# Performance work log

Measured on AMD Instinct MI355X. Metric: run time of the kernel, lower is better.

Reference implementation:

```python
import jax, jax.numpy as jnp
import numpy as np

TEMPERATURE = 0.1
EPS = 1e-12  # matches F.normalize eps clamp


def setup_inputs() -> dict:
    key = jax.random.key(0)
    k1, k2 = jax.random.split(key)
    B, D = 4096, 1024
    z1 = jax.random.normal(k1, (B, D), dtype=jnp.float32)
    z2 = jax.random.normal(k2, (B, D), dtype=jnp.float32)
    return {"z1": z1, "z2": z2}


def reference(z1, z2):
    B = z1.shape[0]
    # L2-normalize rows (F.normalize dim=1, eps clamp)
    n1 = z1 / jnp.maximum(jnp.linalg.norm(z1, axis=1, keepdims=True), EPS)
    n2 = z2 / jnp.maximum(jnp.linalg.norm(z2, axis=1, keepdims=True), EPS)
    reps = jnp.concatenate([n1, n2], axis=0)  # [2B, D]
    # Rows are unit-norm, so cosine similarity == dot product -> one GEMM
    sim = (reps @ reps.T) / TEMPERATURE  # [2B, 2B]
    # positives: diag offsets +B and -B
    pos = jnp.concatenate([jnp.diagonal(sim, B), jnp.diagonal(sim, -B)])  # [2B]
    # logits row i = [pos_i, sim[i, j != i]]. logsumexp over that set =
    # logaddexp(pos_i, logsumexp over the row with the main diagonal removed).
    eye = jnp.eye(2 * B, dtype=bool)
    masked = jnp.where(eye, -jnp.inf, sim)
    lse_neg = jax.scipy.special.logsumexp(masked, axis=1)  # [2B]
    lse = jnp.logaddexp(pos, lse_neg)
    # CrossEntropyLoss with labels==0 -> mean(lse - logit_0) = mean(lse - pos)
    return jnp.mean(lse - pos)
```

## Files before the change

kernel.cpp:

```cpp
#include <hip/hip_runtime.h>

#define D_DIM 1024
#define B_HALF 4096
#define NROWS 8192
#define INV_TEMP 10.0f

typedef __bf16 bf16x8 __attribute__((ext_vector_type(8)));
typedef float floatx4 __attribute__((ext_vector_type(4)));

__device__ __forceinline__ unsigned short f32_to_bf16(float f) {
    union { float f; unsigned u; } v; v.f = f;
    unsigned r = 0x7FFFu + ((v.u >> 16) & 1u);
    return (unsigned short)((v.u + r) >> 16);
}

__global__ __launch_bounds__(256) void normalize_kernel(
    const float* __restrict__ z1, const float* __restrict__ z2,
    unsigned short* __restrict__ R)
{
    const int row = blockIdx.x;
    const int tid = threadIdx.x;
    const float* src = (row < B_HALF) ? (z1 + (size_t)row * D_DIM)
                                      : (z2 + (size_t)(row - B_HALF) * D_DIM);
    float4 v = ((const float4*)src)[tid];
    float ss = v.x * v.x + v.y * v.y + v.z * v.z + v.w * v.w;
    #pragma unroll
    for (int off = 32; off > 0; off >>= 1) ss += __shfl_down(ss, off);
    __shared__ float wsum[4];
    if ((tid & 63) == 0) wsum[tid >> 6] = ss;
    __syncthreads();
    float tot = wsum[0] + wsum[1] + wsum[2] + wsum[3];
    float scale = 1.0f / fmaxf(sqrtf(tot), 1e-12f);
    ushort4 o;
    o.x = f32_to_bf16(v.x * scale);
    o.y = f32_to_bf16(v.y * scale);
    o.z = f32_to_bf16(v.z * scale);
    o.w = f32_to_bf16(v.w * scale);
    ((ushort4*)(R + (size_t)row * D_DIM))[tid] = o;
}

__global__ __launch_bounds__(256) void gemm_lse_kernel(
    const unsigned short* __restrict__ R,
    float* __restrict__ partial, float* __restrict__ pos)
{
    __shared__ unsigned short As[128 * 32];
    __shared__ unsigned short Bs[128 * 32];
    __shared__ float rowsum[2][128];
    __shared__ float colsum[2][128];

    const int t = blockIdx.x;
    int rt = (int)((129.0f - sqrtf((float)(16641 - 8 * t))) * 0.5f);
    while ((rt + 1) * 64 - (rt + 1) * rt / 2 <= t) ++rt;
    while (rt * 64 - rt * (rt - 1) / 2 > t) --rt;
    const int ct = rt + (t - (rt * 64 - rt * (rt - 1) / 2));
    const bool isDiag = (rt == ct);

    const int tid = threadIdx.x;
    const int wave = tid >> 6, lane = tid & 63;
    const int wm = wave >> 1, wn = wave & 1;
    const int row0 = rt * 128, col0 = ct * 128;

    floatx4 acc[4][4] = {};

    const int lrow = lane >> 2;
    const int lk = (lane & 3) * 8;
    const unsigned short* gA = R + (size_t)row0 * D_DIM;
    const unsigned short* gB = R + (size_t)col0 * D_DIM;

    const int lm = lane & 15;
    const int lq = lane >> 4;

    for (int k0 = 0; k0 < D_DIM; k0 += 32) {
        #pragma unroll
        for (int rnd = 0; rnd < 2; ++rnd) {
            const int c = rnd * 4 + wave;
            const int grow = c * 16 + lrow;
            __builtin_amdgcn_global_load_lds(
                (const __attribute__((address_space(1))) unsigned int*)(gA + (size_t)grow * D_DIM + k0 + lk),
                (__attribute__((address_space(3))) unsigned int*)(As + c * 512),
                16, 0, 0);
            __builtin_amdgcn_global_load_lds(
                (const __attribute__((address_space(1))) unsigned int*)(gB + (size_t)grow * D_DIM + k0 + lk),
                (__attribute__((address_space(3))) unsigned int*)(Bs + c * 512),
                16, 0, 0);
        }
        __syncthreads();

        bf16x8 af[4], bfr[4];
        #pragma unroll
        for (int i = 0; i < 4; ++i) {
            af[i]  = *(const bf16x8*)(As + (wm * 64 + i * 16 + lm) * 32 + lq * 8);
            bfr[i] = *(const bf16x8*)(Bs + (wn * 64 + i * 16 + lm) * 32 + lq * 8);
        }
        #pragma unroll
        for (int mi = 0; mi < 4; ++mi)
            #pragma unroll
            for (int ni = 0; ni < 4; ++ni)
                acc[mi][ni] = __builtin_amdgcn_mfma_f32_16x16x32_bf16(
                    af[mi], bfr[ni], acc[mi][ni], 0, 0, 0);
        __syncthreads();
    }

    float ecol[4] = {0.0f, 0.0f, 0.0f, 0.0f};
    #pragma unroll
    for (int mi = 0; mi < 4; ++mi) {
        #pragma unroll
        for (int reg = 0; reg < 4; ++reg) {
            const int gr = row0 + wm * 64 + mi * 16 + lq * 4 + reg;
            float esum = 0.0f;
            #pragma unroll
            for (int ni = 0; ni < 4; ++ni) {
                const int gc = col0 + wn * 64 + ni * 16 + lm;
                float s = acc[mi][ni][reg] * INV_TEMP;
                if (gc == gr + B_HALF) { pos[gr] = s; pos[gc] = s; }
                float e = (gc == gr) ? 0.0f : __expf(s);
                esum += e;
                ecol[ni] += e;
            }
            esum += __shfl_xor(esum, 1);
            esum += __shfl_xor(esum, 2);
            esum += __shfl_xor(esum, 4);
            esum += __shfl_xor(esum, 8);
            if (lm == 0) rowsum[wn][wm * 64 + mi * 16 + lq * 4 + reg] = esum;
        }
    }
    #pragma unroll
    for (int ni = 0; ni < 4; ++ni) {
        ecol[ni] += __shfl_xor(ecol[ni], 16);
        ecol[ni] += __shfl_xor(ecol[ni], 32);
    }
    if (lq == 0 && !isDiag) {
        #pragma unroll
        for (int ni = 0; ni < 4; ++ni)
            colsum[wm][wn * 64 + ni * 16 + lm] = ecol[ni];
    }
    __syncthreads();
    if (tid < 128) {
        partial[(size_t)(row0 + tid) * 64 + ct] = rowsum[0][tid] + rowsum[1][tid];
        if (!isDiag)
            partial[(size_t)(col0 + tid) * 64 + rt] = colsum[0][tid] + colsum[1][tid];
    }
}

__global__ __launch_bounds__(256) void finalize_kernel(
    const float* __restrict__ partial, const float* __restrict__ pos,
    float* __restrict__ out)
{
    const int r = blockIdx.x * 256 + threadIdx.x;
    const float4* p = (const float4*)(partial + (size_t)r * 64);
    float S = 0.0f;
    #pragma unroll
    for (int i = 0; i < 16; ++i) { float4 v = p[i]; S += (v.x + v.y) + (v.z + v.w); }
    const float po = pos[r];
    float contrib = log1pf(S * __expf(-po));
    #pragma unroll
    for (int off = 32; off > 0; off >>= 1) contrib += __shfl_down(contrib, off);
    __shared__ float wsum[4];
    if ((threadIdx.x & 63) == 0) wsum[threadIdx.x >> 6] = contrib;
    __syncthreads();
    if (threadIdx.x == 0)
        atomicAdd(out, (wsum[0] + wsum[1] + wsum[2] + wsum[3]) * (1.0f / 8192.0f));
}

extern "C" void kernel_launch(void* const* d_in, const int* in_sizes, int n_in,
                              void* d_out, int out_size, void* d_ws, size_t ws_size,
                              hipStream_t stream)
{
    const float* z1 = (const float*)d_in[0];
    const float* z2 = (const float*)d_in[1];
    float* out = (float*)d_out;
    char* ws = (char*)d_ws;
    unsigned short* R = (unsigned short*)ws;
    float* partial = (float*)(ws + (size_t)16 * 1024 * 1024);
    float* pos     = (float*)(ws + (size_t)18 * 1024 * 1024);

    hipMemsetAsync(d_out, 0, sizeof(float), stream);
    normalize_kernel<<<NROWS, 256, 0, stream>>>(z1, z2, R);
    gemm_lse_kernel<<<2080, 256, 0, stream>>>(R, partial, pos);
    finalize_kernel<<<32, 256, 0, stream>>>(partial, pos, out);
}
```

Measured before the change: 178.4 us.

## Restructure SimCLR GEMM into 256x256 double-buffered tiles with swizzled LDS

```diff
diff --git a/kernel.cpp b/kernel.cpp
--- a/kernel.cpp
+++ b/kernel.cpp
@@ -4,9 +4,13 @@
 #define B_HALF 4096
 #define NROWS 8192
 #define INV_TEMP 10.0f
+#define NT 32
+#define NKT 16
 
 typedef __bf16 bf16x8 __attribute__((ext_vector_type(8)));
 typedef float floatx4 __attribute__((ext_vector_type(4)));
+
+#define MFMA16 __builtin_amdgcn_mfma_f32_16x16x32_bf16
 
 __device__ __forceinline__ unsigned short f32_to_bf16(float f) {
     union { float f; unsigned u; } v; v.f = f;
@@ -39,74 +43,148 @@
     ((ushort4*)(R + (size_t)row * D_DIM))[tid] = o;
 }
 
-__global__ __launch_bounds__(256) void gemm_lse_kernel(
+__global__ __launch_bounds__(512, 2) void gemm_lse_kernel(
     const unsigned short* __restrict__ R,
     float* __restrict__ partial, float* __restrict__ pos)
 {
-    __shared__ unsigned short As[128 * 32];
-    __shared__ unsigned short Bs[128 * 32];
-    __shared__ float rowsum[2][128];
-    __shared__ float colsum[2][128];
-
-    const int t = blockIdx.x;
-    int rt = (int)((129.0f - sqrtf((float)(16641 - 8 * t))) * 0.5f);
-    while ((rt + 1) * 64 - (rt + 1) * rt / 2 <= t) ++rt;
-    while (rt * 64 - rt * (rt - 1) / 2 > t) --rt;
-    const int ct = rt + (t - (rt * 64 - rt * (rt - 1) / 2));
+    __shared__ unsigned short lds[2][2][256 * 64];
+
+    int t = blockIdx.x;
+    int rt = 0;
+    while (t >= NT - rt) { t -= NT - rt; ++rt; }
+    const int ct = rt + t;
     const bool isDiag = (rt == ct);
 
     const int tid = threadIdx.x;
     const int wave = tid >> 6, lane = tid & 63;
-    const int wm = wave >> 1, wn = wave & 1;
-    const int row0 = rt * 128, col0 = ct * 128;
-
-    floatx4 acc[4][4] = {};
-
-    const int lrow = lane >> 2;
-    const int lk = (lane & 3) * 8;
-    const unsigned short* gA = R + (size_t)row0 * D_DIM;
-    const unsigned short* gB = R + (size_t)col0 * D_DIM;
-
-    const int lm = lane & 15;
-    const int lq = lane >> 4;
-
-    for (int k0 = 0; k0 < D_DIM; k0 += 32) {
-        #pragma unroll
-        for (int rnd = 0; rnd < 2; ++rnd) {
-            const int c = rnd * 4 + wave;
-            const int grow = c * 16 + lrow;
-            __builtin_amdgcn_global_load_lds(
-                (const __attribute__((address_space(1))) unsigned int*)(gA + (size_t)grow * D_DIM + k0 + lk),
-                (__attribute__((address_space(3))) unsigned int*)(As + c * 512),
-                16, 0, 0);
-            __builtin_amdgcn_global_load_lds(
-                (const __attribute__((address_space(1))) unsigned int*)(gB + (size_t)grow * D_DIM + k0 + lk),
-                (__attribute__((address_space(3))) unsigned int*)(Bs + c * 512),
-                16, 0, 0);
-        }
-        __syncthreads();
-
-        bf16x8 af[4], bfr[4];
-        #pragma unroll
-        for (int i = 0; i < 4; ++i) {
-            af[i]  = *(const bf16x8*)(As + (wm * 64 + i * 16 + lm) * 32 + lq * 8);
-            bfr[i] = *(const bf16x8*)(Bs + (wn * 64 + i * 16 + lm) * 32 + lq * 8);
-        }
-        #pragma unroll
-        for (int mi = 0; mi < 4; ++mi)
-            #pragma unroll
-            for (int ni = 0; ni < 4; ++ni)
-                acc[mi][ni] = __builtin_amdgcn_mfma_f32_16x16x32_bf16(
-                    af[mi], bfr[ni], acc[mi][ni], 0, 0, 0);
-        __syncthreads();
-    }
+    const int wm = wave >> 2, wn = wave & 3;
+    const int row0 = rt * 256, col0 = ct * 256;
+    const int lm = lane & 15, lq = lane >> 4;
+
+    const unsigned short* __restrict__ gA = R + (size_t)row0 * D_DIM;
+    const unsigned short* __restrict__ gB = R + (size_t)col0 * D_DIM;
+
+    const int sRow  = lane >> 3;
+    const int sSlot = (lane & 7) ^ sRow;
+    const int aOff = (wm * 128 + lm) * 64;
+    const int bOff = (wn * 64 + lm) * 64;
+    const int sk0 = ((0 + lq) ^ (lm & 7)) * 8;
+    const int sk1 = ((4 + lq) ^ (lm & 7)) * 8;
+
+    floatx4 acc[8][4] = {};
+
+#define STAGE_A(dstbuf, kk) \
+    { _Pragma("unroll") \
+      for (int i = 0; i < 4; ++i) \
+        __builtin_amdgcn_global_load_lds( \
+          (const __attribute__((address_space(1))) unsigned int*)(gA + (size_t)(i * 64 + wave * 8 + sRow) * D_DIM + (kk) + sSlot * 8), \
+          (__attribute__((address_space(3))) unsigned int*)(&lds[dstbuf][0][(i * 64 + wave * 8) * 64]), \
+          16, 0, 0); }
+
+#define STAGE_B(dstbuf, kk) \
+    { _Pragma("unroll") \
+      for (int i = 0; i < 4; ++i) \
+        __builtin_amdgcn_global_load_lds( \
+          (const __attribute__((address_space(1))) unsigned int*)(gB + (size_t)(i * 64 + wave * 8 + sRow) * D_DIM + (kk) + sSlot * 8), \
+          (__attribute__((address_space(3))) unsigned int*)(&lds[dstbuf][1][(i * 64 + wave * 8) * 64]), \
+          16, 0, 0); }
+
+    STAGE_A(0, 0)
+    STAGE_B(0, 0)
+    asm volatile("s_waitcnt vmcnt(0)" ::: "memory");
+    __builtin_amdgcn_s_barrier();
+
+    bf16x8 a[4][2];
+    bf16x8 b[2][2][2];
+
+    for (int kt = 0; kt < NKT; ++kt) {
+        const int buf = kt & 1;
+        const unsigned short* As = &lds[buf][0][0];
+        const unsigned short* Bs = &lds[buf][1][0];
+        const int kn = (kt + 1) * 64;
+        const bool more = (kt + 1 < NKT);
+
+        if (more) STAGE_A(buf ^ 1, kn)
+        #pragma unroll
+        for (int mi = 0; mi < 4; ++mi) {
+            a[mi][0] = *(const bf16x8*)(As + aOff + mi * 1024 + sk0);
+            a[mi][1] = *(const bf16x8*)(As + aOff + mi * 1024 + sk1);
+        }
+        #pragma unroll
+        for (int ni = 0; ni < 2; ++ni) {
+            b[0][ni][0] = *(const bf16x8*)(Bs + bOff + ni * 1024 + sk0);
+            b[0][ni][1] = *(const bf16x8*)(Bs + bOff + ni * 1024 + sk1);
+        }
+        __builtin_amdgcn_s_barrier();
+        __builtin_amdgcn_s_setprio(1);
+        #pragma unroll
+        for (int mi = 0; mi < 4; ++mi)
+            #pragma unroll
+            for (int ni = 0; ni < 2; ++ni) {
+                acc[mi][ni] = MFMA16(a[mi][0], b[0][ni][0], acc[mi][ni], 0, 0, 0);
+                acc[mi][ni] = MFMA16(a[mi][1], b[0][ni][1], acc[mi][ni], 0, 0, 0);
+            }
+        __builtin_amdgcn_s_setprio(0);
+        __builtin_amdgcn_s_barrier();
+
+        if (more) STAGE_B(buf ^ 1, kn)
+        #pragma unroll
+        for (int ni = 0; ni < 2; ++ni) {
+            b[1][ni][0] = *(const bf16x8*)(Bs + bOff + (2 + ni) * 1024 + sk0);
+            b[1][ni][1] = *(const bf16x8*)(Bs + bOff + (2 + ni) * 1024 + sk1);
+        }
+        __builtin_amdgcn_s_barrier();
+        __builtin_amdgcn_s_setprio(1);
+        #pragma unroll
+        for (int mi = 0; mi < 4; ++mi)
+            #pragma unroll
+            for (int ni = 0; ni < 2; ++ni) {
+                acc[mi][2 + ni] = MFMA16(a[mi][0], b[1][ni][0], acc[mi][2 + ni], 0, 0, 0);
+                acc[mi][2 + ni] = MFMA16(a[mi][1], b[1][ni][1], acc[mi][2 + ni], 0, 0, 0);
+            }
+        __builtin_amdgcn_s_setprio(0);
+        __builtin_amdgcn_s_barrier();
+
+        #pragma unroll
+        for (int mi = 0; mi < 4; ++mi) {
+            a[mi][0] = *(const bf16x8*)(As + aOff + (4 + mi) * 1024 + sk0);
+            a[mi][1] = *(const bf16x8*)(As + aOff + (4 + mi) * 1024 + sk1);
+        }
+        __builtin_amdgcn_s_barrier();
+        __builtin_amdgcn_s_setprio(1);
+        #pragma unroll
+        for (int mi = 0; mi < 4; ++mi)
+            #pragma unroll
+            for (int ni = 0; ni < 2; ++ni) {
+                acc[4 + mi][ni] = MFMA16(a[mi][0], b[0][ni][0], acc[4 + mi][ni], 0, 0, 0);
+                acc[4 + mi][ni] = MFMA16(a[mi][1], b[0][ni][1], acc[4 + mi][ni], 0, 0, 0);
+            }
+        __builtin_amdgcn_s_setprio(0);
+        __builtin_amdgcn_s_barrier();
+
+        __builtin_amdgcn_s_setprio(1);
+        #pragma unroll
+        for (int mi = 0; mi < 4; ++mi)
+            #pragma unroll
+            for (int ni = 0; ni < 2; ++ni) {
+                acc[4 + mi][2 + ni] = MFMA16(a[mi][0], b[1][ni][0], acc[4 + mi][2 + ni], 0, 0, 0);
+                acc[4 + mi][2 + ni] = MFMA16(a[mi][1], b[1][ni][1], acc[4 + mi][2 + ni], 0, 0, 0);
+            }
+        __builtin_amdgcn_s_setprio(0);
+        asm volatile("s_waitcnt vmcnt(0)" ::: "memory");
+        __builtin_amdgcn_s_barrier();
+        asm volatile("" ::: "memory");
+    }
+
+    float* rowsum = (float*)&lds[0][0][0];
+    float* colsum = rowsum + 4 * 256;
 
     float ecol[4] = {0.0f, 0.0f, 0.0f, 0.0f};
     #pragma unroll
-    for (int mi = 0; mi < 4; ++mi) {
+    for (int mi = 0; mi < 8; ++mi) {
         #pragma unroll
         for (int reg = 0; reg < 4; ++reg) {
-            const int gr = row0 + wm * 64 + mi * 16 + lq * 4 + reg;
+            const int gr = row0 + wm * 128 + mi * 16 + lq * 4 + reg;
             float esum = 0.0f;
             #pragma unroll
             for (int ni = 0; ni < 4; ++ni) {
@@ -121,7 +199,7 @@
             esum += __shfl_xor(esum, 2);
             esum += __shfl_xor(esum, 4);
             esum += __shfl_xor(esum, 8);
-            if (lm == 0) rowsum[wn][wm * 64 + mi * 16 + lq * 4 + reg] = esum;
+            if (lm == 0) rowsum[wn * 256 + wm * 128 + mi * 16 + lq * 4 + reg] = esum;
         }
     }
     #pragma unroll
@@ -132,13 +210,17 @@
     if (lq == 0 && !isDiag) {
         #pragma unroll
         for (int ni = 0; ni < 4; ++ni)
-            colsum[wm][wn * 64 + ni * 16 + lm] = ecol[ni];
+            colsum[wm * 256 + wn * 64 + ni * 16 + lm] = ecol[ni];
     }
     __syncthreads();
-    if (tid < 128) {
-        partial[(size_t)(row0 + tid) * 64 + ct] = rowsum[0][tid] + rowsum[1][tid];
-        if (!isDiag)
-            partial[(size_t)(col0 + tid) * 64 + rt] = colsum[0][tid] + colsum[1][tid];
+    if (tid < 256) {
+        float rs = rowsum[0 * 256 + tid] + rowsum[1 * 256 + tid]
+                 + rowsum[2 * 256 + tid] + rowsum[3 * 256 + tid];
+        partial[(size_t)(row0 + tid) * NT + ct] = rs;
+        if (!isDiag) {
+            float cs = colsum[0 * 256 + tid] + colsum[1 * 256 + tid];
+            partial[(size_t)(col0 + tid) * NT + rt] = cs;
+        }
     }
 }
 
@@ -147,10 +229,10 @@
     float* __restrict__ out)
 {
     const int r = blockIdx.x * 256 + threadIdx.x;
-    const float4* p = (const float4*)(partial + (size_t)r * 64);
+    const float4* p = (const float4*)(partial + (size_t)r * NT);
     float S = 0.0f;
     #pragma unroll
-    for (int i = 0; i < 16; ++i) { float4 v = p[i]; S += (v.x + v.y) + (v.z + v.w); }
+    for (int i = 0; i < 8; ++i) { float4 v = p[i]; S += (v.x + v.y) + (v.z + v.w); }
     const float po = pos[r];
     float contrib = log1pf(S * __expf(-po));
     #pragma unroll
@@ -176,6 +258,6 @@
 
     hipMemsetAsync(d_out, 0, sizeof(float), stream);
     normalize_kernel<<<NROWS, 256, 0, stream>>>(z1, z2, R);
-    gemm_lse_kernel<<<2080, 256, 0, stream>>>(R, partial, pos);
+    gemm_lse_kernel<<<528, 512, 0, stream>>>(R, partial, pos);
     finalize_kernel<<<32, 256, 0, stream>>>(partial, pos, out);
 }
```

Result: no change. 181.9 us (+2.0%).
